# Kernel optimization log

Measured on AMD Instinct MI355X. Metric: run time of the kernel, lower is better.

## Reference

```python
import jax, jax.numpy as jnp
import numpy as np

N = 20000
E = 640000
D = 128


def setup_inputs() -> dict:
    key = jax.random.key(0)
    ks = jax.random.split(key, 8)
    x = jax.random.normal(ks[0], (N, D), dtype=jnp.float32)
    edge_index = jax.random.randint(ks[1], (2, E), 0, N, dtype=jnp.int64)
    s = 1.0 / np.sqrt(D)
    inp = {"x": x, "edge_index": edge_index}
    for i, layer in enumerate([2, 4, 6]):
        inp[f"W{i+1}"] = jax.random.uniform(ks[layer], (D, D), jnp.float32, -s, s)
        inp[f"b{i+1}"] = jax.random.uniform(ks[layer + 1], (D,), jnp.float32, -s, s)
    return inp


def _gcn_layer(x, src, dst, deg_inv, W, b):
    # linear (torch convention: y = x @ W.T + b), W: [out, in]
    xt = x @ W.T + b
    # gather source-node features, scatter-mean onto targets
    msg = xt[src]                                   # [E, D]
    agg = jax.ops.segment_sum(msg, dst, num_segments=N)  # [N, D]
    agg = agg * deg_inv[:, None]                    # mean over incoming edges
    return jax.nn.relu(agg) + xt


def reference(x, edge_index, W1, b1, W2, b2, W3, b3):
    src, dst = edge_index[0], edge_index[1]
    deg = jax.ops.segment_sum(jnp.ones((E,), jnp.float32), dst, num_segments=N)
    deg_inv = jnp.where(deg > 0, 1.0 / jnp.maximum(deg, 1.0), 0.0)
    for W, b in ((W1, b1), (W2, b2), (W3, b3)):
        x = _gcn_layer(x, src, dst, deg_inv, W, b)
    return x
```

## Files before the change

kernel.cpp:

```cpp
#include <hip/hip_runtime.h>

#define DD 128
#define KC 32
#define MT 64
#define ELLC 128
#define NBMAX 320
#define ACAP 2304
#define AEPW 4096

__device__ __forceinline__ unsigned f2bf_rne(float f) {
    unsigned u = __float_as_uint(f);
    u += 0x7fffu + ((u >> 16) & 1u);
    return u >> 16;
}

__device__ __forceinline__ void gemm_body(float Xs[KC][MT + 4], float Ws[KC][DD + 4],
                                          const float* x,
                                          const float* __restrict__ W,
                                          const float* __restrict__ b,
                                          float* xt,
                                          unsigned* __restrict__ xtb, int M, int blk) {
    const int tid  = threadIdx.x;
    const int cg   = tid & 15;
    const int rg   = tid >> 4;
    const int row0 = blk * MT;

    float acc[4][8];
#pragma unroll
    for (int i = 0; i < 4; ++i)
#pragma unroll
        for (int j = 0; j < 8; ++j) acc[i][j] = 0.0f;

    for (int kc = 0; kc < DD; kc += KC) {
#pragma unroll
        for (int it = 0; it < 2; ++it) {
            int idx = tid + it * 256;
            int r = idx >> 3, kq = idx & 7;
            int gr = row0 + r;
            float4 v = make_float4(0.f, 0.f, 0.f, 0.f);
            if (gr < M) v = *(const float4*)&x[gr * DD + kc + kq * 4];
            Xs[kq * 4 + 0][r] = v.x; Xs[kq * 4 + 1][r] = v.y;
            Xs[kq * 4 + 2][r] = v.z; Xs[kq * 4 + 3][r] = v.w;
        }
#pragma unroll
        for (int it = 0; it < 4; ++it) {
            int idx = tid + it * 256;
            int o = idx >> 3, kq = idx & 7;
            float4 v = *(const float4*)&W[o * DD + kc + kq * 4];
            Ws[kq * 4 + 0][o] = v.x; Ws[kq * 4 + 1][o] = v.y;
            Ws[kq * 4 + 2][o] = v.z; Ws[kq * 4 + 3][o] = v.w;
        }
        __syncthreads();

#pragma unroll 8
        for (int k = 0; k < KC; ++k) {
            float4 xv = *(const float4*)&Xs[k][rg * 4];
            float4 w0 = *(const float4*)&Ws[k][cg * 8];
            float4 w1 = *(const float4*)&Ws[k][cg * 8 + 4];
            float xr[4] = {xv.x, xv.y, xv.z, xv.w};
            float wc[8] = {w0.x, w0.y, w0.z, w0.w, w1.x, w1.y, w1.z, w1.w};
#pragma unroll
            for (int i = 0; i < 4; ++i)
#pragma unroll
                for (int j = 0; j < 8; ++j) acc[i][j] += xr[i] * wc[j];
        }
        __syncthreads();
    }

    float4 b0 = *(const float4*)&b[cg * 8];
    float4 b1 = *(const float4*)&b[cg * 8 + 4];
    float bb[8] = {b0.x, b0.y, b0.z, b0.w, b1.x, b1.y, b1.z, b1.w};
#pragma unroll
    for (int i = 0; i < 4; ++i) {
        int gr = row0 + rg * 4 + i;
        if (gr < M) {
            float v[8];
#pragma unroll
            for (int j = 0; j < 8; ++j) v[j] = acc[i][j] + bb[j];
            *(float4*)&xt[gr * DD + cg * 8]     = make_float4(v[0], v[1], v[2], v[3]);
            *(float4*)&xt[gr * DD + cg * 8 + 4] = make_float4(v[4], v[5], v[6], v[7]);
            uint4 p;
            p.x = f2bf_rne(v[0]) | (f2bf_rne(v[1]) << 16);
            p.y = f2bf_rne(v[2]) | (f2bf_rne(v[3]) << 16);
            p.z = f2bf_rne(v[4]) | (f2bf_rne(v[5]) << 16);
            p.w = f2bf_rne(v[6]) | (f2bf_rne(v[7]) << 16);
            *(uint4*)&xtb[gr * 64 + cg * 4] = p;
        }
    }
}

__global__ __launch_bounds__(256) void gemm_xwT(const float* x,
                                                const float* __restrict__ W,
                                                const float* __restrict__ b,
                                                float* xt,
                                                unsigned* __restrict__ xtb, int M) {
    __shared__ float Xs[KC][MT + 4];
    __shared__ float Ws[KC][DD + 4];
    gemm_body(Xs, Ws, x, W, b, xt, xtb, M, blockIdx.x);
}

__global__ __launch_bounds__(256) void gemm1_plus_binA(const float* x,
                                                       const float* __restrict__ W,
                                                       const float* __restrict__ b,
                                                       float* xt,
                                                       unsigned* __restrict__ xtb, int M,
                                                       const int* __restrict__ src,
                                                       const int* __restrict__ dst,
                                                       int* __restrict__ bucket_count,
                                                       unsigned* __restrict__ bstore,
                                                       int E, int NB, int PA) {
    __shared__ float Xs[KC][MT + 4];
    __shared__ float Ws[KC][DD + 4];
    __shared__ int hist[NBMAX];
    __shared__ int basec[NBMAX];
    __shared__ int cur[NBMAX];

    if ((int)blockIdx.x >= PA) {
        gemm_body(Xs, Ws, x, W, b, xt, xtb, M, blockIdx.x - PA);
        return;
    }

    const int tid = threadIdx.x;
    for (int i = tid; i < NB; i += 256) hist[i] = 0;
    __syncthreads();

    int dv[16], sv[16];
    const int ebase = blockIdx.x * AEPW;
#pragma unroll
    for (int r = 0; r < 4; ++r) {
        int e = ebase + r * 1024 + tid * 4;
        if (e + 4 <= E) {
            int4 d4 = *(const int4*)&dst[e];
            int4 s4 = *(const int4*)&src[e];
            dv[r*4+0] = d4.x; dv[r*4+1] = d4.y; dv[r*4+2] = d4.z; dv[r*4+3] = d4.w;
            sv[r*4+0] = s4.x; sv[r*4+1] = s4.y; sv[r*4+2] = s4.z; sv[r*4+3] = s4.w;
        } else {
#pragma unroll
            for (int q = 0; q < 4; ++q) {
                int ee = e + q;
                if (ee < E) { dv[r*4+q] = dst[ee]; sv[r*4+q] = src[ee]; }
                else        { dv[r*4+q] = -1;      sv[r*4+q] = 0; }
            }
        }
    }
#pragma unroll
    for (int i = 0; i < 16; ++i)
        if (dv[i] >= 0) atomicAdd(&hist[dv[i] >> 6], 1);
    __syncthreads();

    for (int bk = tid; bk < NB; bk += 256) {
        int h = hist[bk];
        basec[bk] = h ? atomicAdd(&bucket_count[bk], h) : 0;
        cur[bk] = 0;
    }
    __syncthreads();

#pragma unroll
    for (int i = 0; i < 16; ++i) {
        if (dv[i] >= 0) {
            int bk = dv[i] >> 6;
            int pos = basec[bk] + atomicAdd(&cur[bk], 1);
            if (pos < ACAP)
                bstore[bk * ACAP + pos] = ((unsigned)(dv[i] & 63) << 16) | (unsigned)sv[i];
        }
    }
}

__global__ __launch_bounds__(256) void ell_build(const unsigned* __restrict__ bstore,
                                                 const int* __restrict__ bucket_count,
                                                 unsigned short* __restrict__ colell,
                                                 int* __restrict__ deg, int N) {
    __shared__ int c64[64];
    const int bk = blockIdx.x;
    for (int i = threadIdx.x; i < 64; i += 256) c64[i] = 0;
    __syncthreads();
    int cnt = bucket_count[bk];
    if (cnt > ACAP) cnt = ACAP;
    for (int i = threadIdx.x; i < cnt; i += 256) {
        unsigned code = bstore[bk * ACAP + i];
        int local = (int)(code >> 16);
        int s     = (int)(code & 0xffffu);
        int p = atomicAdd(&c64[local], 1);
        if (p < ELLC)
            colell[((((bk << 6) + local)) << 7) + p] = (unsigned short)s;
    }
    __syncthreads();
    if (threadIdx.x < 64) {
        int node = (bk << 6) + threadIdx.x;
        if (node < N) deg[node] = c64[threadIdx.x];
    }
}

__global__ void gcn_aggregate(const uint2* __restrict__ xtb2, const float* xt,
                              const unsigned short* __restrict__ colell,
                              const int* __restrict__ deg,
                              float* out, int N) {
    const int gid  = blockIdx.x * blockDim.x + threadIdx.x;
    const int node = gid >> 6;
    const int lane = threadIdx.x & 63;
    if (node >= N) return;
    const int h    = lane & 31;
    const int half = lane >> 5;

    const uint2* __restrict__ xl = xtb2 + h;
    const unsigned short* __restrict__ crow = colell + (node << 7);
    const int cnt = deg[node];

    float a0 = 0.f, a1 = 0.f, a2 = 0.f, a3 = 0.f;

    for (int base = 0; base < cnt; base += 64) {
        const int rem = cnt - base;
        const int c = rem < 64 ? rem : 64;
        const int myidx = (lane < c) ? (int)crow[base + lane] : 0;
        const int pairs = c >> 1;
        int t = 0;
        for (; t + 8 <= pairs; t += 8) {
            uint2 u[8];
#pragma unroll
            for (int q = 0; q < 8; ++q) {
                int s = __shfl(myidx, 2 * (t + q) + half, 64);
                u[q] = xl[s << 5];
            }
#pragma unroll
            for (int q = 0; q < 8; ++q) {
                a0 += __uint_as_float(u[q].x << 16);
                a1 += __uint_as_float(u[q].x & 0xffff0000u);
                a2 += __uint_as_float(u[q].y << 16);
                a3 += __uint_as_float(u[q].y & 0xffff0000u);
            }
        }
        for (; t < pairs; ++t) {
            int s = __shfl(myidx, 2 * t + half, 64);
            uint2 u = xl[s << 5];
            a0 += __uint_as_float(u.x << 16);
            a1 += __uint_as_float(u.x & 0xffff0000u);
            a2 += __uint_as_float(u.y << 16);
            a3 += __uint_as_float(u.y & 0xffff0000u);
        }
        if (c & 1) {
            int s = __shfl(myidx, c - 1, 64);
            if (half == 0) {
                uint2 u = xl[s << 5];
                a0 += __uint_as_float(u.x << 16);
                a1 += __uint_as_float(u.x & 0xffff0000u);
                a2 += __uint_as_float(u.y << 16);
                a3 += __uint_as_float(u.y & 0xffff0000u);
            }
        }
    }

    a0 += __shfl_down(a0, 32, 64);
    a1 += __shfl_down(a1, 32, 64);
    a2 += __shfl_down(a2, 32, 64);
    a3 += __shfl_down(a3, 32, 64);

    if (half == 0) {
        const float di = (cnt > 0) ? (1.0f / (float)cnt) : 0.0f;
        float4 t4 = ((const float4*)xt)[node * 32 + h];
        float4 o;
        o.x = fmaxf(a0 * di, 0.f) + t4.x;
        o.y = fmaxf(a1 * di, 0.f) + t4.y;
        o.z = fmaxf(a2 * di, 0.f) + t4.z;
        o.w = fmaxf(a3 * di, 0.f) + t4.w;
        ((float4*)out)[node * 32 + h] = o;
    }
}

extern "C" void kernel_launch(void* const* d_in, const int* in_sizes, int n_in,
                              void* d_out, int out_size, void* d_ws, size_t ws_size,
                              hipStream_t stream) {
    const float* x  = (const float*)d_in[0];
    const int*   ei = (const int*)d_in[1];
    const float* W1 = (const float*)d_in[2];
    const float* b1 = (const float*)d_in[3];
    const float* W2 = (const float*)d_in[4];
    const float* b2 = (const float*)d_in[5];
    const float* W3 = (const float*)d_in[6];
    const float* b3 = (const float*)d_in[7];

    const int N  = in_sizes[0] / DD;
    const int E  = in_sizes[1] / 2;
    const int ND = N * DD;

    const int* src = ei;
    const int* dst = ei + E;

    const int NB = (N + 63) >> 6;
    const int PA = (E + AEPW - 1) / AEPW;
    const int GB = (N + MT - 1) / MT;
    const int AB = (N + 3) / 4;

    char* ws = (char*)d_ws;
    size_t off = 0;
    auto alloc = [&](size_t bytes) {
        void* p = ws + off;
        off += (bytes + 255) & ~(size_t)255;
        return p;
    };
    int*            bucket_count = (int*)alloc((size_t)NB * sizeof(int));
    unsigned*       bstore       = (unsigned*)alloc((size_t)NB * ACAP * sizeof(unsigned));
    unsigned short* colell       = (unsigned short*)alloc((size_t)NB * 64 * ELLC * sizeof(unsigned short));
    int*            deg          = (int*)alloc((size_t)N * sizeof(int));
    unsigned*       xtb          = (unsigned*)alloc((size_t)(ND / 2) * sizeof(unsigned));

    float* xbuf = (float*)d_out;

    hipMemsetAsync(bucket_count, 0, (size_t)NB * sizeof(int), stream);
    gemm1_plus_binA<<<PA + GB, 256, 0, stream>>>(x, W1, b1, xbuf, xtb, N,
                                                 src, dst, bucket_count, bstore, E, NB, PA);
    ell_build<<<NB, 256, 0, stream>>>(bstore, bucket_count, colell, deg, N);

    gcn_aggregate<<<AB, 256, 0, stream>>>((const uint2*)xtb, xbuf, colell, deg, xbuf, N);

    gemm_xwT<<<GB, 256, 0, stream>>>(xbuf, W2, b2, xbuf, xtb, N);
    gcn_aggregate<<<AB, 256, 0, stream>>>((const uint2*)xtb, xbuf, colell, deg, xbuf, N);

    gemm_xwT<<<GB, 256, 0, stream>>>(xbuf, W3, b3, xbuf, xtb, N);
    gcn_aggregate<<<AB, 256, 0, stream>>>((const uint2*)xtb, xbuf, colell, deg, xbuf, N);
}
```

Baseline: 212.8 us.

## Split bf16 features into two column planes with XCD-aware aggregation mapping

Stores the bf16 copy of the transformed features as two 64-column planes, padded with a zero sentinel row. Block indices are mapped so each XCD group works on one plane, which halves the gathered footprint each XCD's L2 must hold. The aggregation kernel now uses 16 lanes per row and 4 edges per step. Neighbour lists are padded to multiples of 16 with the sentinel node so the tail handling goes away. The cost is twice as many aggregation waves, each reading half rows, plus an extra cross-lane reduction step.

```diff
diff --git a/kernel.cpp b/kernel.cpp
--- a/kernel.cpp
+++ b/kernel.cpp
@@ -19,7 +19,7 @@
                                           const float* __restrict__ W,
                                           const float* __restrict__ b,
                                           float* xt,
-                                          unsigned* __restrict__ xtb, int M, int blk) {
+                                          unsigned* __restrict__ xtb, int M, int PS, int blk) {
     const int tid  = threadIdx.x;
     const int cg   = tid & 15;
     const int rg   = tid >> 4;
@@ -84,7 +84,9 @@
             p.y = f2bf_rne(v[2]) | (f2bf_rne(v[3]) << 16);
             p.z = f2bf_rne(v[4]) | (f2bf_rne(v[5]) << 16);
             p.w = f2bf_rne(v[6]) | (f2bf_rne(v[7]) << 16);
-            *(uint4*)&xtb[gr * 64 + cg * 4] = p;
+            unsigned* xp = xtb + (size_t)(cg >> 3) * ((size_t)PS * 32)
+                               + (size_t)gr * 32 + ((cg & 7) << 2);
+            *(uint4*)xp = p;
         }
     }
 }
@@ -93,17 +95,17 @@
                                                 const float* __restrict__ W,
                                                 const float* __restrict__ b,
                                                 float* xt,
-                                                unsigned* __restrict__ xtb, int M) {
+                                                unsigned* __restrict__ xtb, int M, int PS) {
     __shared__ float Xs[KC][MT + 4];
     __shared__ float Ws[KC][DD + 4];
-    gemm_body(Xs, Ws, x, W, b, xt, xtb, M, blockIdx.x);
+    gemm_body(Xs, Ws, x, W, b, xt, xtb, M, PS, blockIdx.x);
 }
 
 __global__ __launch_bounds__(256) void gemm1_plus_binA(const float* x,
                                                        const float* __restrict__ W,
                                                        const float* __restrict__ b,
                                                        float* xt,
-                                                       unsigned* __restrict__ xtb, int M,
+                                                       unsigned* __restrict__ xtb, int M, int PS,
                                                        const int* __restrict__ src,
                                                        const int* __restrict__ dst,
                                                        int* __restrict__ bucket_count,
@@ -116,7 +118,7 @@
     __shared__ int cur[NBMAX];
 
     if ((int)blockIdx.x >= PA) {
-        gemm_body(Xs, Ws, x, W, b, xt, xtb, M, blockIdx.x - PA);
+        gemm_body(Xs, Ws, x, W, b, xt, xtb, M, PS, blockIdx.x - PA);
         return;
     }
 
@@ -169,7 +171,9 @@
 __global__ __launch_bounds__(256) void ell_build(const unsigned* __restrict__ bstore,
                                                  const int* __restrict__ bucket_count,
                                                  unsigned short* __restrict__ colell,
-                                                 int* __restrict__ deg, int N) {
+                                                 int* __restrict__ deg,
+                                                 unsigned* __restrict__ xtb,
+                                                 int PS, int N) {
     __shared__ int c64[64];
     const int bk = blockIdx.x;
     for (int i = threadIdx.x; i < 64; i += 256) c64[i] = 0;
@@ -187,82 +191,94 @@
     __syncthreads();
     if (threadIdx.x < 64) {
         int node = (bk << 6) + threadIdx.x;
-        if (node < N) deg[node] = c64[threadIdx.x];
-    }
-}
-
-__global__ void gcn_aggregate(const uint2* __restrict__ xtb2, const float* xt,
-                              const unsigned short* __restrict__ colell,
-                              const int* __restrict__ deg,
-                              float* out, int N) {
-    const int gid  = blockIdx.x * blockDim.x + threadIdx.x;
-    const int node = gid >> 6;
-    const int lane = threadIdx.x & 63;
+        if (node < N) {
+            int d = c64[threadIdx.x];
+            deg[node] = d;
+            int stored = d < ELLC ? d : ELLC;
+            int padded = (stored + 15) & ~15;
+            if (padded > ELLC) padded = ELLC;
+            unsigned short* row = colell + ((size_t)node << 7);
+            for (int p2 = stored; p2 < padded; ++p2) row[p2] = (unsigned short)N;
+        }
+    }
+    if (bk == 0 && threadIdx.x >= 64 && threadIdx.x < 80) {
+        int i  = threadIdx.x - 64;
+        int pl = i >> 3;
+        int j  = i & 7;
+        *(uint4*)&xtb[((size_t)pl * PS + (size_t)N) * 32 + (size_t)j * 4] =
+            make_uint4(0u, 0u, 0u, 0u);
+    }
+}
+
+__global__ __launch_bounds__(256) void gcn_aggregate(const uint2* __restrict__ xtb2,
+                                                     const float* xt,
+                                                     const unsigned short* __restrict__ colell,
+                                                     const int* __restrict__ deg,
+                                                     float* out, int PS, int N) {
+    const int wave  = threadIdx.x >> 6;
+    const int lane  = threadIdx.x & 63;
+    const int xcd   = blockIdx.x & 7;
+    const int plane = xcd >> 2;
+    const int widx  = ((blockIdx.x >> 3) << 2) | (xcd & 3);
+    const int node  = (widx << 2) | wave;
     if (node >= N) return;
-    const int h    = lane & 31;
-    const int half = lane >> 5;
-
-    const uint2* __restrict__ xl = xtb2 + h;
-    const unsigned short* __restrict__ crow = colell + (node << 7);
+    const int h = lane & 15;
+    const int q = lane >> 4;
+
+    const uint2* __restrict__ xl = xtb2 + (size_t)plane * ((size_t)PS << 4) + h;
+    const unsigned short* __restrict__ crow = colell + ((size_t)node << 7);
     const int cnt = deg[node];
+    const int cl  = cnt < ELLC ? cnt : ELLC;
 
     float a0 = 0.f, a1 = 0.f, a2 = 0.f, a3 = 0.f;
 
-    for (int base = 0; base < cnt; base += 64) {
-        const int rem = cnt - base;
+#define GATH(u_, j_) { int s_ = __shfl(myidx, ((t + (j_)) << 2) | q, 64); \
+                       (u_)[j_] = xl[(size_t)s_ << 4]; }
+#define UNPK(u_, j_) { a0 += __uint_as_float((u_)[j_].x << 16); \
+                       a1 += __uint_as_float((u_)[j_].x & 0xffff0000u); \
+                       a2 += __uint_as_float((u_)[j_].y << 16); \
+                       a3 += __uint_as_float((u_)[j_].y & 0xffff0000u); }
+
+    for (int base = 0; base < cl; base += 64) {
+        const int rem = cl - base;
         const int c = rem < 64 ? rem : 64;
-        const int myidx = (lane < c) ? (int)crow[base + lane] : 0;
-        const int pairs = c >> 1;
+        const int myidx = (int)crow[base + lane];
+        const int cq = ((c + 15) >> 4) << 2;
         int t = 0;
-        for (; t + 8 <= pairs; t += 8) {
+        for (; t + 8 <= cq; t += 8) {
             uint2 u[8];
-#pragma unroll
-            for (int q = 0; q < 8; ++q) {
-                int s = __shfl(myidx, 2 * (t + q) + half, 64);
-                u[q] = xl[s << 5];
-            }
-#pragma unroll
-            for (int q = 0; q < 8; ++q) {
-                a0 += __uint_as_float(u[q].x << 16);
-                a1 += __uint_as_float(u[q].x & 0xffff0000u);
-                a2 += __uint_as_float(u[q].y << 16);
-                a3 += __uint_as_float(u[q].y & 0xffff0000u);
-            }
-        }
-        for (; t < pairs; ++t) {
-            int s = __shfl(myidx, 2 * t + half, 64);
-            uint2 u = xl[s << 5];
-            a0 += __uint_as_float(u.x << 16);
-            a1 += __uint_as_float(u.x & 0xffff0000u);
-            a2 += __uint_as_float(u.y << 16);
-            a3 += __uint_as_float(u.y & 0xffff0000u);
-        }
-        if (c & 1) {
-            int s = __shfl(myidx, c - 1, 64);
-            if (half == 0) {
-                uint2 u = xl[s << 5];
-                a0 += __uint_as_float(u.x << 16);
-                a1 += __uint_as_float(u.x & 0xffff0000u);
-                a2 += __uint_as_float(u.y << 16);
-                a3 += __uint_as_float(u.y & 0xffff0000u);
-            }
-        }
-    }
+            GATH(u,0) GATH(u,1) GATH(u,2) GATH(u,3)
+            GATH(u,4) GATH(u,5) GATH(u,6) GATH(u,7)
+            UNPK(u,0) UNPK(u,1) UNPK(u,2) UNPK(u,3)
+            UNPK(u,4) UNPK(u,5) UNPK(u,6) UNPK(u,7)
+        }
+        if (t < cq) {
+            uint2 u[4];
+            GATH(u,0) GATH(u,1) GATH(u,2) GATH(u,3)
+            UNPK(u,0) UNPK(u,1) UNPK(u,2) UNPK(u,3)
+        }
+    }
+#undef GATH
+#undef UNPK
 
     a0 += __shfl_down(a0, 32, 64);
     a1 += __shfl_down(a1, 32, 64);
     a2 += __shfl_down(a2, 32, 64);
     a3 += __shfl_down(a3, 32, 64);
-
-    if (half == 0) {
+    a0 += __shfl_down(a0, 16, 64);
+    a1 += __shfl_down(a1, 16, 64);
+    a2 += __shfl_down(a2, 16, 64);
+    a3 += __shfl_down(a3, 16, 64);
+
+    if (q == 0) {
         const float di = (cnt > 0) ? (1.0f / (float)cnt) : 0.0f;
-        float4 t4 = ((const float4*)xt)[node * 32 + h];
+        float4 t4 = ((const float4*)xt)[(size_t)node * 32 + plane * 16 + h];
         float4 o;
         o.x = fmaxf(a0 * di, 0.f) + t4.x;
         o.y = fmaxf(a1 * di, 0.f) + t4.y;
         o.z = fmaxf(a2 * di, 0.f) + t4.z;
         o.w = fmaxf(a3 * di, 0.f) + t4.w;
-        ((float4*)out)[node * 32 + h] = o;
+        ((float4*)out)[(size_t)node * 32 + plane * 16 + h] = o;
     }
 }
 
@@ -280,7 +296,7 @@
 
     const int N  = in_sizes[0] / DD;
     const int E  = in_sizes[1] / 2;
-    const int ND = N * DD;
+    const int PS = N + 1;
 
     const int* src = ei;
     const int* dst = ei + E;
@@ -288,7 +304,8 @@
     const int NB = (N + 63) >> 6;
     const int PA = (E + AEPW - 1) / AEPW;
     const int GB = (N + MT - 1) / MT;
-    const int AB = (N + 3) / 4;
+    const int SUP = (N + 15) >> 4;
+    const int AGB = SUP * 8;
 
     char* ws = (char*)d_ws;
     size_t off = 0;
@@ -301,20 +318,20 @@
     unsigned*       bstore       = (unsigned*)alloc((size_t)NB * ACAP * sizeof(unsigned));
     unsigned short* colell       = (unsigned short*)alloc((size_t)NB * 64 * ELLC * sizeof(unsigned short));
     int*            deg          = (int*)alloc((size_t)N * sizeof(int));
-    unsigned*       xtb          = (unsigned*)alloc((size_t)(ND / 2) * sizeof(unsigned));
+    unsigned*       xtb          = (unsigned*)alloc((size_t)PS * 256);
 
     float* xbuf = (float*)d_out;
 
     hipMemsetAsync(bucket_count, 0, (size_t)NB * sizeof(int), stream);
-    gemm1_plus_binA<<<PA + GB, 256, 0, stream>>>(x, W1, b1, xbuf, xtb, N,
+    gemm1_plus_binA<<<PA + GB, 256, 0, stream>>>(x, W1, b1, xbuf, xtb, N, PS,
                                                  src, dst, bucket_count, bstore, E, NB, PA);
-    ell_build<<<NB, 256, 0, stream>>>(bstore, bucket_count, colell, deg, N);
-
-    gcn_aggregate<<<AB, 256, 0, stream>>>((const uint2*)xtb, xbuf, colell, deg, xbuf, N);
-
-    gemm_xwT<<<GB, 256, 0, stream>>>(xbuf, W2, b2, xbuf, xtb, N);
-    gcn_aggregate<<<AB, 256, 0, stream>>>((const uint2*)xtb, xbuf, colell, deg, xbuf, N);
-
-    gemm_xwT<<<GB, 256, 0, stream>>>(xbuf, W3, b3, xbuf, xtb, N);
-    gcn_aggregate<<<AB, 256, 0, stream>>>((const uint2*)xtb, xbuf, colell, deg, xbuf, N);
-}
+    ell_build<<<NB, 256, 0, stream>>>(bstore, bucket_count, colell, deg, xtb, PS, N);
+
+    gcn_aggregate<<<AGB, 256, 0, stream>>>((const uint2*)xtb, xbuf, colell, deg, xbuf, PS, N);
+
+    gemm_xwT<<<GB, 256, 0, stream>>>(xbuf, W2, b2, xbuf, xtb, N, PS);
+    gcn_aggregate<<<AGB, 256, 0, stream>>>((const uint2*)xtb, xbuf, colell, deg, xbuf, PS, N);
+
+    gemm_xwT<<<GB, 256, 0, stream>>>(xbuf, W3, b3, xbuf, xtb, N, PS);
+    gcn_aggregate<<<AGB, 256, 0, stream>>>((const uint2*)xtb, xbuf, colell, deg, xbuf, PS, N);
+}
```

After: 213.5 us. About the same (+0.3%).
